# Optimization experiments

Measured on AMD Instinct MI355X. Metric: run time of the kernel, lower is better.

The kernel has to match this reference:

```python
import jax, jax.numpy as jnp
import numpy as np

DIM = 256
NUM_HEADS = 4
HEAD_DIM = DIM // NUM_HEADS


def setup_inputs() -> dict:
    key = jax.random.key(0)
    ks = jax.random.split(key, 8)
    B, N, C = 4, 2048, DIM
    x = jax.random.normal(ks[0], (B, N, C), dtype=jnp.float32)
    R = jax.random.normal(ks[1], (B, 3, 3), dtype=jnp.float32)
    P = jax.random.normal(ks[2], (N, 3), dtype=jnp.float32)
    s = 1.0 / np.sqrt(C)
    qkv_w = jax.random.normal(ks[3], (3 * C, C), dtype=jnp.float32) * s
    qkv_b = jax.random.normal(ks[4], (3 * C,), dtype=jnp.float32) * 0.02
    proj_w = jax.random.normal(ks[5], (C, C), dtype=jnp.float32) * s
    proj_b = jax.random.normal(ks[6], (C,), dtype=jnp.float32) * 0.02
    pos_scale = jnp.asarray(1.0, dtype=jnp.float32)
    return {"x": x, "R": R, "P": P, "qkv_w": qkv_w, "qkv_b": qkv_b,
            "proj_w": proj_w, "proj_b": proj_b, "pos_scale": pos_scale}


def reference(x, R, P, qkv_w, qkv_b, proj_w, proj_b, pos_scale):
    B, N, C = x.shape
    H, D = NUM_HEADS, HEAD_DIM
    scale = D ** -0.5
    # qkv: (B,N,3C) -> (3,B,H,N,D)
    qkv = (x @ qkv_w.T + qkv_b).reshape(B, N, 3, H, D).transpose(2, 0, 3, 1, 4)
    q, k, v = qkv[0], qkv[1], qkv[2]
    # attention logits (B,H,N,N)
    attn = jnp.einsum('bhid,bhjd->bhij', q, k) * scale
    # positional bias: RP = (R @ P^T)^T -> (B,N,3); bias_ij = dot(RP_i, P_j)
    RP = jnp.einsum('bab,jb->bja', R, P) if False else jnp.einsum('bca,ja->bjc', jnp.swapaxes(R, 1, 2), P)
    RP = jnp.einsum('bcd,jd->bjc', R, P)  # (B,N,3): (R @ P.T).T
    bias = jnp.einsum('bik,jk->bij', RP, P)[:, None, :, :] * pos_scale  # (B,1,N,N) broadcast over heads
    attn = jax.nn.softmax(attn + bias, axis=-1)
    out = jnp.einsum('bhij,bhjd->bhid', attn, v)  # (B,H,N,D)
    out = out.transpose(0, 2, 1, 3).reshape(B, N, C)
    out = out @ proj_w.T + proj_b
    return out
```

## Files before the change

### kernel.cpp

```cpp
#include <hip/hip_runtime.h>
#include <hip/hip_bf16.h>

#define B_ 4
#define N_ 2048
#define C_ 256
#define H_ 4
#define D_ 64

typedef __attribute__((ext_vector_type(8))) short bf16x8;
typedef __attribute__((ext_vector_type(4))) float f32x4;

#define LOG2E 1.4426950408889634f

static __device__ inline unsigned short f2bf(float f) {
    unsigned u = __builtin_bit_cast(unsigned, f);
    unsigned r = (u + 0x7fffu + ((u >> 16) & 1u)) >> 16;
    return (unsigned short)r;
}
static __device__ inline float bf2f(unsigned short h) {
    unsigned u = ((unsigned)h) << 16;
    return __builtin_bit_cast(float, u);
}
static __device__ inline unsigned pack2(float a, float b) {
    __hip_bfloat162 h = __float22bfloat162_rn(make_float2(a, b));
    unsigned u;
    __builtin_memcpy(&u, &h, 4);
    return u;
}
static __device__ inline bf16x8 ld_frag(const unsigned short* p) {
    return __builtin_bit_cast(bf16x8, *(const uint4*)p);
}
static __device__ inline void gload_lds16(const unsigned short* g, unsigned short* l) {
    __builtin_amdgcn_global_load_lds(
        (const __attribute__((address_space(1))) unsigned int*)(g),
        (__attribute__((address_space(3))) unsigned int*)(l),
        16, 0, 0);
}
template<int CTRL>
static __device__ inline float fmax_dpp(float x) {
    int yi = __builtin_amdgcn_update_dpp(0, __builtin_bit_cast(int, x),
                                         CTRL, 0xf, 0xf, true);
    return fmaxf(x, __builtin_bit_cast(float, yi));
}

__global__ __launch_bounds__(256) void cvt_kernel(
    const float* __restrict__ x, const float* __restrict__ qkv_w,
    const float* __restrict__ proj_w, const float* __restrict__ Pm,
    unsigned short* __restrict__ xb, unsigned short* __restrict__ wqb,
    unsigned short* __restrict__ wpb, unsigned short* __restrict__ eb)
{
    const int bid = blockIdx.x, tid = threadIdx.x;
    if (bid >= 1152) {
        const int n = (bid - 1152) * 256 + tid;
        const float* pp = Pm + n * 3;
        float p0 = pp[0], p1 = pp[1], p2 = pp[2];
        unsigned u0 = f2bf(p0), u1 = f2bf(p1), u2 = f2bf(p2);
        unsigned v0 = f2bf(p0 - bf2f((unsigned short)u0));
        unsigned v1 = f2bf(p1 - bf2f((unsigned short)u1));
        unsigned v2 = f2bf(p2 - bf2f((unsigned short)u2));
        uint4 lo, hi;
        lo.x = u0 | (u1 << 16); lo.y = u2 | (v0 << 16);
        lo.z = v1 | (v2 << 16); lo.w = u0 | (u1 << 16);
        hi.x = u2; hi.y = 0u; hi.z = 0u; hi.w = 0u;
        *(uint4*)&eb[n * 16 + 0] = lo;
        *(uint4*)&eb[n * 16 + 8] = hi;
        return;
    }
    const float* s; unsigned short* d; int i;
    if (bid < 1024)      { s = x;      d = xb;  i = (bid * 256 + tid) * 8; }
    else if (bid < 1120) { s = qkv_w;  d = wqb; i = ((bid - 1024) * 256 + tid) * 8; }
    else                 { s = proj_w; d = wpb; i = ((bid - 1120) * 256 + tid) * 8; }
    float4 a = *(const float4*)(s + i);
    float4 b = *(const float4*)(s + i + 4);
    uint4 u;
    u.x = pack2(a.x, a.y); u.y = pack2(a.z, a.w);
    u.z = pack2(b.x, b.y); u.w = pack2(b.z, b.w);
    *(uint4*)(d + i) = u;
}

__global__ __launch_bounds__(256) void qkv_gemm(
    const unsigned short* __restrict__ xb, const unsigned short* __restrict__ wb,
    const float* __restrict__ bias, unsigned short* __restrict__ qb,
    unsigned short* __restrict__ kb, unsigned short* __restrict__ vt)
{
    __shared__ __align__(16) unsigned short As[128 * 40];
    __shared__ __align__(16) unsigned short Bs[128 * 40];
    const int m0 = blockIdx.x * 128, o0 = blockIdx.y * 128;
    const int tid = threadIdx.x;
    const int wave = tid >> 6, lane = tid & 63, quad = lane >> 4, l16 = lane & 15;
    const int wy = wave >> 1, wx = wave & 1;

    f32x4 acc[4][4];
    #pragma unroll
    for (int i = 0; i < 4; ++i)
        #pragma unroll
        for (int j = 0; j < 4; ++j) acc[i][j] = (f32x4){0.f, 0.f, 0.f, 0.f};

    const int srow = tid >> 1, soff = (tid & 1) * 16;

    for (int k0 = 0; k0 < 256; k0 += 32) {
        __syncthreads();
        {
            const unsigned short* sa = &xb[(size_t)(m0 + srow) * 256 + k0 + soff];
            const unsigned short* sb = &wb[(size_t)(o0 + srow) * 256 + k0 + soff];
            *(uint4*)&As[srow * 40 + soff + 0] = *(const uint4*)(sa + 0);
            *(uint4*)&As[srow * 40 + soff + 8] = *(const uint4*)(sa + 8);
            *(uint4*)&Bs[srow * 40 + soff + 0] = *(const uint4*)(sb + 0);
            *(uint4*)&Bs[srow * 40 + soff + 8] = *(const uint4*)(sb + 8);
        }
        __syncthreads();
        bf16x8 a[4], b[4];
        #pragma unroll
        for (int mt = 0; mt < 4; ++mt) a[mt] = ld_frag(&As[(wy * 64 + mt * 16 + l16) * 40 + quad * 8]);
        #pragma unroll
        for (int nt = 0; nt < 4; ++nt) b[nt] = ld_frag(&Bs[(wx * 64 + nt * 16 + l16) * 40 + quad * 8]);
        #pragma unroll
        for (int mt = 0; mt < 4; ++mt)
            #pragma unroll
            for (int nt = 0; nt < 4; ++nt)
                acc[mt][nt] = __builtin_amdgcn_mfma_f32_16x16x32_bf16(a[mt], b[nt], acc[mt][nt], 0, 0, 0);
    }

    const int sec = o0 + wx * 64;
    const int three = sec >> 8;
    const int h = (sec >> 6) & 3;
    const int b = m0 >> 11;
    float bv[4];
    #pragma unroll
    for (int nt = 0; nt < 4; ++nt) bv[nt] = bias[sec + nt * 16 + l16];

    if (three == 2) {
        const int n64 = (m0 + wy * 64) & 2047;
        const size_t bh64 = ((size_t)b * H_ + h) * 64;
        #pragma unroll
        for (int nt = 0; nt < 4; ++nt) {
            int d = nt * 16 + l16;
            #pragma unroll
            for (int r = 0; r < 4; ++r) {
                ushort4 v;
                v.x = f2bf(acc[0][nt][r] + bv[nt]);
                v.y = f2bf(acc[1][nt][r] + bv[nt]);
                v.z = f2bf(acc[2][nt][r] + bv[nt]);
                v.w = f2bf(acc[3][nt][r] + bv[nt]);
                *(ushort4*)&vt[(bh64 + d) * N_ + n64 + 16 * quad + 4 * r] = v;
            }
        }
    } else {
        unsigned short* dst = (three == 0) ? qb : kb;
        float sc = (three == 0) ? (0.125f * LOG2E) : 1.0f;
        #pragma unroll
        for (int mt = 0; mt < 4; ++mt)
            #pragma unroll
            for (int r = 0; r < 4; ++r) {
                int n = (m0 + wy * 64 + mt * 16 + quad * 4 + r) & 2047;
                size_t rowbase = (((size_t)b * H_ + h) * N_ + n) * D_;
                #pragma unroll
                for (int nt = 0; nt < 4; ++nt)
                    dst[rowbase + nt * 16 + l16] = f2bf((acc[mt][nt][r] + bv[nt]) * sc);
            }
    }
}

#define LDK 64

__global__ __launch_bounds__(256) void attn_kernel(
    const unsigned short* __restrict__ qb, const unsigned short* __restrict__ kb,
    const unsigned short* __restrict__ vt, const unsigned short* __restrict__ eb,
    const float* __restrict__ Rm, const float* __restrict__ Pm,
    const float* __restrict__ ps_ptr,
    unsigned short* __restrict__ Opart, float* __restrict__ ml)
{
    __shared__ __align__(16) unsigned short Ks[2][64 * LDK];
    __shared__ __align__(16) unsigned short Vs[2][64 * LDK];
    __shared__ __align__(16) unsigned short Ps[64 * LDK];

    const int bh = blockIdx.y;
    const int b = bh >> 2;
    const int i0 = blockIdx.x * 64;
    const int split = blockIdx.z;
    const int tid = threadIdx.x;
    const int wave = tid >> 6, lane = tid & 63;
    const int quad = lane >> 4, l16 = lane & 15;
    const int x7 = l16 & 7;
    const float ps = ps_ptr[0];

    const size_t base = (size_t)bh * N_ * D_;
    const unsigned short* qg = qb + base;
    const unsigned short* kg = kb + base;
    const unsigned short* vg = vt + base;

    const int jbeg = split * (N_ / 4);

    const int rl = lane >> 3, sl = lane & 7;
    const int swz = (sl ^ rl) * 8;
    const unsigned short* kq = kg + (size_t)(jbeg + wave * 16 + rl) * D_ + swz;
    const unsigned short* vq = vg + (size_t)(wave * 16 + rl) * N_ + jbeg + swz;
    const unsigned short* ep = eb + (size_t)(jbeg + l16) * 16 + (quad & 1) * 8;

    auto ISSUE_K = [&](int nb) {
        unsigned short* kd = &Ks[nb][(wave * 16) * LDK];
        gload_lds16(kq,          kd);
        gload_lds16(kq + 8 * D_, kd + 8 * LDK);
        kq += 64 * D_;
    };
    auto ISSUE_V = [&](int nb) {
        unsigned short* vd = &Vs[nb][(wave * 16) * LDK];
        gload_lds16(vq,          vd);
        gload_lds16(vq + 8 * N_, vd + 8 * LDK);
        vq += 64;
    };
    auto LOAD_E = [&](bf16x8 (&e)[4]) {
        #pragma unroll
        for (int t = 0; t < 4; ++t) e[t] = ld_frag(ep + t * 256);
        ep += 64 * 16;
    };

    ISSUE_K(0);
    bf16x8 eA[4], eB[4];
    LOAD_E(eA);

    const int qrow = i0 + wave * 16 + l16;
    bf16x8 aq[3];
    #pragma unroll
    for (int ks = 0; ks < 2; ++ks)
        aq[ks] = ld_frag(&qg[(size_t)qrow * D_ + ks * 32 + quad * 8]);

    {
        float p0 = Pm[qrow * 3 + 0], p1 = Pm[qrow * 3 + 1], p2 = Pm[qrow * 3 + 2];
        float sc = ps * LOG2E;
        unsigned short ah[3], al[3];
        #pragma unroll
        for (int c = 0; c < 3; ++c) {
            float a = (Rm[b * 9 + c * 3 + 0] * p0 + Rm[b * 9 + c * 3 + 1] * p1
                     + Rm[b * 9 + c * 3 + 2] * p2) * sc;
            ah[c] = f2bf(a);
            al[c] = f2bf(a - bf2f(ah[c]));
        }
        bf16x8 e = (bf16x8){0,0,0,0,0,0,0,0};
        if (quad == 0) {
            e[0] = (short)ah[0]; e[1] = (short)ah[1]; e[2] = (short)ah[2];
            e[3] = (short)ah[0]; e[4] = (short)ah[1]; e[5] = (short)ah[2];
            e[6] = (short)al[0]; e[7] = (short)al[1];
        } else if (quad == 1) {
            e[0] = (short)al[2];
        }
        aq[2] = e;
    }

    const bf16x8 ones = (bf16x8){0x3F80,0x3F80,0x3F80,0x3F80,0x3F80,0x3F80,0x3F80,0x3F80};

    float m_run = -1e30f;
    f32x4 o_acc[4], lacc;
    #pragma unroll
    for (int t = 0; t < 4; ++t) o_acc[t] = (f32x4){0.f, 0.f, 0.f, 0.f};
    lacc = (f32x4){0.f, 0.f, 0.f, 0.f};

    f32x4 sA[4], sB[4];

    auto S_COMPUTE = [&](f32x4 (&sc)[4], int kb_, bf16x8 (&ec)[4]) {
        __builtin_amdgcn_s_setprio(1);
        #pragma unroll
        for (int t = 0; t < 4; ++t) {
            const int rb = (l16 + 16 * t) * LDK;
            f32x4 c = {0.f, 0.f, 0.f, 0.f};
            #pragma unroll
            for (int ks = 0; ks < 2; ++ks) {
                bf16x8 bk = ld_frag(&Ks[kb_][rb + (((ks * 4 + quad) ^ x7) * 8)]);
                c = __builtin_amdgcn_mfma_f32_16x16x32_bf16(aq[ks], bk, c, 0, 0, 0);
            }
            c = __builtin_amdgcn_mfma_f32_16x16x32_bf16(aq[2], ec[t], c, 0, 0, 0);
            sc[t] = c;
        }
        __builtin_amdgcn_s_setprio(0);
    };

    auto SOFTMAX = [&](f32x4 (&s)[4]) {
        float mt[4];
        #pragma unroll
        for (int t = 0; t < 4; ++t)
            mt[t] = fmaxf(fmaxf(s[t][0], s[t][1]), fmaxf(s[t][2], s[t][3]));
        float mx = fmaxf(fmaxf(mt[0], mt[1]), fmaxf(mt[2], mt[3]));
        mx = fmax_dpp<0xB1>(mx);
        mx = fmax_dpp<0x4E>(mx);
        mx = fmax_dpp<0x124>(mx);
        mx = fmax_dpp<0x128>(mx);
        if (__any(mx > m_run + 8.0f)) {
            float mnew = fmaxf(m_run, mx);
            float alpha = exp2f(m_run - mnew);
            #pragma unroll
            for (int t = 0; t < 4; ++t)
                #pragma unroll
                for (int r = 0; r < 4; ++r)
                    o_acc[t][r] *= alpha;
            #pragma unroll
            for (int r = 0; r < 4; ++r) lacc[r] *= alpha;
            m_run = mnew;
        }
        #pragma unroll
        for (int r = 0; r < 4; ++r) {
            float p0 = exp2f(s[0][r] - m_run), p1 = exp2f(s[1][r] - m_run);
            float p2 = exp2f(s[2][r] - m_run), p3 = exp2f(s[3][r] - m_run);
            uint2 w;
            w.x = pack2(p0, p1);
            w.y = pack2(p2, p3);
            const int prow = quad * 4 + r;
            *(uint2*)&Ps[(wave * 16 + prow) * LDK
                         + (((l16 >> 1) ^ (prow & 7)) * 8) + (l16 & 1) * 4] = w;
        }
    };

    auto PV = [&](int vb_) {
        __builtin_amdgcn_s_setprio(1);
        #pragma unroll
        for (int ks = 0; ks < 2; ++ks) {
            bf16x8 ap = ld_frag(&Ps[(wave * 16 + l16) * LDK
                                    + (((ks * 4 + quad) ^ x7) * 8)]);
            #pragma unroll
            for (int t = 0; t < 4; ++t) {
                bf16x8 bv = ld_frag(&Vs[vb_][(l16 + 16 * t) * LDK
                                             + (((ks * 4 + quad) ^ x7) * 8)]);
                o_acc[t] = __builtin_amdgcn_mfma_f32_16x16x32_bf16(ap, bv, o_acc[t], 0, 0, 0);
            }
            lacc = __builtin_amdgcn_mfma_f32_16x16x32_bf16(ap, ones, lacc, 0, 0, 0);
        }
        __builtin_amdgcn_s_setprio(0);
    };

    auto STEP = [&](int cur, bool more, f32x4 (&snew)[4], f32x4 (&sold)[4],
                    bf16x8 (&euse)[4], bf16x8 (&eload)[4]) {
        asm volatile("s_waitcnt vmcnt(0)" ::: "memory");
        __builtin_amdgcn_s_barrier();
        __builtin_amdgcn_sched_barrier(0);
        if (more) ISSUE_K(cur ^ 1);
        ISSUE_V(cur);
        SOFTMAX(sold);
        S_COMPUTE(snew, cur, euse);
        if (more) LOAD_E(eload);
        PV(cur ^ 1);
    };

    asm volatile("s_waitcnt vmcnt(0)" ::: "memory");
    __builtin_amdgcn_s_barrier();
    __builtin_amdgcn_sched_barrier(0);
    ISSUE_K(1);
    ISSUE_V(0);
    S_COMPUTE(sA, 0, eA);
    LOAD_E(eB);

    #pragma unroll 1
    for (int it = 0; it < 3; ++it) {
        STEP(1, true, sB, sA, eB, eA);
        STEP(0, true, sA, sB, eA, eB);
    }
    STEP(1, false, sB, sA, eB, eA);

    asm volatile("s_waitcnt vmcnt(0)" ::: "memory");
    __builtin_amdgcn_s_barrier();
    __builtin_amdgcn_sched_barrier(0);
    SOFTMAX(sB);
    PV(1);

    const size_t pbase = (size_t)(split * 16 + bh) * N_;
    #pragma unroll
    for (int r = 0; r < 4; ++r) {
        int row = i0 + wave * 16 + quad * 4 + r;
        #pragma unroll
        for (int t = 0; t < 4; ++t)
            Opart[(pbase + row) * D_ + l16 + 16 * t] = f2bf(o_acc[t][r]);
        if (l16 == 0) {
            float2* mlp = (float2*)ml;
            mlp[pbase + row] = make_float2(m_run, lacc[r]);
        }
    }
}

__global__ __launch_bounds__(256) void proj_gemm(
    const unsigned short* __restrict__ Opart, const float* __restrict__ ml,
    const unsigned short* __restrict__ wb, const float* __restrict__ bias,
    float* __restrict__ out)
{
    __shared__ __align__(16) unsigned short As[64 * 40];
    __shared__ __align__(16) unsigned short Bs[64 * 40];
    const int m0 = blockIdx.x * 64, o0 = blockIdx.y * 64;
    const int tid = threadIdx.x;
    const int wave = tid >> 6, lane = tid & 63, quad = lane >> 4, l16 = lane & 15;
    const float2* mlp = (const float2*)ml;

    const int srow = tid >> 2, scb = (tid & 3) * 8;
    const int sm = m0 + srow, sb = sm >> 11, sn = sm & 2047;

    float wgt[4][4];
    #pragma unroll
    for (int h = 0; h < 4; ++h) {
        size_t r1 = (size_t)(sb * 4 + h) * N_ + sn;
        float2 m0v = mlp[r1], m1v = mlp[r1 + 16 * N_];
        float2 m2v = mlp[r1 + 32 * N_], m3v = mlp[r1 + 48 * N_];
        float mm = fmaxf(fmaxf(m0v.x, m1v.x), fmaxf(m2v.x, m3v.x));
        float w0 = exp2f(m0v.x - mm), w1 = exp2f(m1v.x - mm);
        float w2 = exp2f(m2v.x - mm), w3 = exp2f(m3v.x - mm);
        float inv = 1.f / (m0v.y * w0 + m1v.y * w1 + m2v.y * w2 + m3v.y * w3);
        wgt[h][0] = w0 * inv; wgt[h][1] = w1 * inv;
        wgt[h][2] = w2 * inv; wgt[h][3] = w3 * inv;
    }

    f32x4 acc[4];
    #pragma unroll
    for (int j = 0; j < 4; ++j) acc[j] = (f32x4){0.f, 0.f, 0.f, 0.f};

    for (int k0 = 0; k0 < 256; k0 += 32) {
        const int h = k0 >> 6;
        const int d0 = (k0 & 63) + scb;
        __syncthreads();
        {
            size_t r1 = (size_t)(sb * 4 + h) * N_ + sn;
            union { uint4 u; unsigned short s[8]; } a0, a1, a2, a3;
            a0.u = *(const uint4*)&Opart[(r1 +  0 * N_) * D_ + d0];
            a1.u = *(const uint4*)&Opart[(r1 + 16 * N_) * D_ + d0];
            a2.u = *(const uint4*)&Opart[(r1 + 32 * N_) * D_ + d0];
            a3.u = *(const uint4*)&Opart[(r1 + 48 * N_) * D_ + d0];
            float w0 = wgt[h][0], w1 = wgt[h][1], w2 = wgt[h][2], w3 = wgt[h][3];
            uint4 mv;
            unsigned* mp = (unsigned*)&mv;
            #pragma unroll
            for (int j = 0; j < 4; ++j) {
                float lo = bf2f(a0.s[2*j]) * w0 + bf2f(a1.s[2*j]) * w1
                         + bf2f(a2.s[2*j]) * w2 + bf2f(a3.s[2*j]) * w3;
                float hi = bf2f(a0.s[2*j+1]) * w0 + bf2f(a1.s[2*j+1]) * w1
                         + bf2f(a2.s[2*j+1]) * w2 + bf2f(a3.s[2*j+1]) * w3;
                mp[j] = pack2(lo, hi);
            }
            *(uint4*)&As[srow * 40 + scb] = mv;
            *(uint4*)&Bs[srow * 40 + scb] = *(const uint4*)&wb[(size_t)(o0 + srow) * 256 + k0 + scb];
        }
        __syncthreads();
        bf16x8 a = ld_frag(&As[(wave * 16 + l16) * 40 + quad * 8]);
        #pragma unroll
        for (int nt = 0; nt < 4; ++nt) {
            bf16x8 b = ld_frag(&Bs[(nt * 16 + l16) * 40 + quad * 8]);
            acc[nt] = __builtin_amdgcn_mfma_f32_16x16x32_bf16(a, b, acc[nt], 0, 0, 0);
        }
    }

    float bv[4];
    #pragma unroll
    for (int nt = 0; nt < 4; ++nt) bv[nt] = bias[o0 + nt * 16 + l16];
    #pragma unroll
    for (int r = 0; r < 4; ++r) {
        int m = m0 + wave * 16 + quad * 4 + r;
        #pragma unroll
        for (int nt = 0; nt < 4; ++nt)
            out[(size_t)m * 256 + o0 + nt * 16 + l16] = acc[nt][r] + bv[nt];
    }
}

extern "C" void kernel_launch(void* const* d_in, const int* in_sizes, int n_in,
                              void* d_out, int out_size, void* d_ws, size_t ws_size,
                              hipStream_t stream) {
    const float* x       = (const float*)d_in[0];
    const float* Rm      = (const float*)d_in[1];
    const float* Pm      = (const float*)d_in[2];
    const float* qkv_w   = (const float*)d_in[3];
    const float* qkv_b   = (const float*)d_in[4];
    const float* proj_w  = (const float*)d_in[5];
    const float* proj_b  = (const float*)d_in[6];
    const float* pos_scl = (const float*)d_in[7];
    float* out = (float*)d_out;

    const size_t NE = (size_t)B_ * H_ * N_ * D_;
    unsigned short* opart = (unsigned short*)d_ws;
    unsigned short* qb    = opart + 4 * NE;
    unsigned short* kb    = qb   + NE;
    unsigned short* vtb   = kb   + NE;
    float*          mlb   = (float*)(vtb + NE);
    unsigned short* eb    = (unsigned short*)(mlb + (size_t)4 * 16 * N_ * 2);
    unsigned short* wqb   = eb  + 2048 * 16;
    unsigned short* wpb   = wqb + 768 * 256;
    unsigned short* xb    = opart;

    cvt_kernel<<<1160, 256, 0, stream>>>(x, qkv_w, proj_w, Pm, xb, wqb, wpb, eb);
    qkv_gemm<<<dim3(64, 6), 256, 0, stream>>>(xb, wqb, qkv_b, qb, kb, vtb);
    attn_kernel<<<dim3(32, 16, 4), 256, 0, stream>>>(qb, kb, vtb, eb, Rm, Pm, pos_scl, opart, mlb);
    proj_gemm<<<dim3(128, 4), 256, 0, stream>>>(opart, mlb, wpb, proj_b, out);
}
```

Before: 136.2 us.

## Double-buffer QKV and projection GEMMs with direct-to-LDS loads and XOR swizzle

Rewrites the K loops of the QKV and output-projection GEMMs to use double-buffered shared memory with a K step of 64. Tiles are fetched via global-to-LDS direct loads into an XOR-swizzled layout, so the next tile's fetch overlaps MFMA work on the current one and bank conflicts are avoided. The projection kernel also prefetches the next head's partial outputs into registers. The cost is double the LDS footprint and more register pressure, and the gains are limited to the two GEMM stages; the attention kernel is untouched.

New measurement: 134.3 us. Within noise of the previous version (-1.4%).

```diff
diff --git a/kernel.cpp b/kernel.cpp
--- a/kernel.cpp
+++ b/kernel.cpp
@@ -83,12 +83,28 @@
     const float* __restrict__ bias, unsigned short* __restrict__ qb,
     unsigned short* __restrict__ kb, unsigned short* __restrict__ vt)
 {
-    __shared__ __align__(16) unsigned short As[128 * 40];
-    __shared__ __align__(16) unsigned short Bs[128 * 40];
+    __shared__ __align__(16) unsigned short As[2][128 * 64];
+    __shared__ __align__(16) unsigned short Bs[2][128 * 64];
     const int m0 = blockIdx.x * 128, o0 = blockIdx.y * 128;
     const int tid = threadIdx.x;
     const int wave = tid >> 6, lane = tid & 63, quad = lane >> 4, l16 = lane & 15;
     const int wy = wave >> 1, wx = wave & 1;
+    const int x7 = l16 & 7;
+    const int rl = lane >> 3, sl = lane & 7;
+    const int swz = (sl ^ rl) * 8;
+
+    const unsigned short* aq0 = &xb[(size_t)(m0 + 32 * wave + rl) * 256 + swz];
+    const unsigned short* bq0 = &wb[(size_t)(o0 + 32 * wave + rl) * 256 + swz];
+
+    auto ISSUE = [&](int buf, int k0) {
+        unsigned short* ad = &As[buf][(32 * wave) * 64];
+        unsigned short* bd = &Bs[buf][(32 * wave) * 64];
+        #pragma unroll
+        for (int i = 0; i < 4; ++i) {
+            gload_lds16(aq0 + (size_t)(8 * i) * 256 + k0, ad + (8 * i) * 64);
+            gload_lds16(bq0 + (size_t)(8 * i) * 256 + k0, bd + (8 * i) * 64);
+        }
+    };
 
     f32x4 acc[4][4];
     #pragma unroll
@@ -96,29 +112,34 @@
         #pragma unroll
         for (int j = 0; j < 4; ++j) acc[i][j] = (f32x4){0.f, 0.f, 0.f, 0.f};
 
-    const int srow = tid >> 1, soff = (tid & 1) * 16;
-
-    for (int k0 = 0; k0 < 256; k0 += 32) {
-        __syncthreads();
-        {
-            const unsigned short* sa = &xb[(size_t)(m0 + srow) * 256 + k0 + soff];
-            const unsigned short* sb = &wb[(size_t)(o0 + srow) * 256 + k0 + soff];
-            *(uint4*)&As[srow * 40 + soff + 0] = *(const uint4*)(sa + 0);
-            *(uint4*)&As[srow * 40 + soff + 8] = *(const uint4*)(sa + 8);
-            *(uint4*)&Bs[srow * 40 + soff + 0] = *(const uint4*)(sb + 0);
-            *(uint4*)&Bs[srow * 40 + soff + 8] = *(const uint4*)(sb + 8);
-        }
-        __syncthreads();
-        bf16x8 a[4], b[4];
-        #pragma unroll
-        for (int mt = 0; mt < 4; ++mt) a[mt] = ld_frag(&As[(wy * 64 + mt * 16 + l16) * 40 + quad * 8]);
-        #pragma unroll
-        for (int nt = 0; nt < 4; ++nt) b[nt] = ld_frag(&Bs[(wx * 64 + nt * 16 + l16) * 40 + quad * 8]);
-        #pragma unroll
-        for (int mt = 0; mt < 4; ++mt)
+    ISSUE(0, 0);
+
+    #pragma unroll
+    for (int t = 0; t < 4; ++t) {
+        const int cur = t & 1;
+        asm volatile("s_waitcnt vmcnt(0)" ::: "memory");
+        __builtin_amdgcn_s_barrier();
+        __builtin_amdgcn_sched_barrier(0);
+        if (t < 3) ISSUE(cur ^ 1, (t + 1) * 64);
+        __builtin_amdgcn_s_setprio(1);
+        #pragma unroll
+        for (int ks = 0; ks < 2; ++ks) {
+            bf16x8 a[4], b[4];
+            #pragma unroll
+            for (int mt = 0; mt < 4; ++mt)
+                a[mt] = ld_frag(&As[cur][(wy * 64 + mt * 16 + l16) * 64
+                                         + (((ks * 4 + quad) ^ x7) * 8)]);
             #pragma unroll
             for (int nt = 0; nt < 4; ++nt)
-                acc[mt][nt] = __builtin_amdgcn_mfma_f32_16x16x32_bf16(a[mt], b[nt], acc[mt][nt], 0, 0, 0);
+                b[nt] = ld_frag(&Bs[cur][(wx * 64 + nt * 16 + l16) * 64
+                                         + (((ks * 4 + quad) ^ x7) * 8)]);
+            #pragma unroll
+            for (int mt = 0; mt < 4; ++mt)
+                #pragma unroll
+                for (int nt = 0; nt < 4; ++nt)
+                    acc[mt][nt] = __builtin_amdgcn_mfma_f32_16x16x32_bf16(a[mt], b[nt], acc[mt][nt], 0, 0, 0);
+        }
+        __builtin_amdgcn_s_setprio(0);
     }
 
     const int sec = o0 + wx * 64;
@@ -379,14 +400,18 @@
     const unsigned short* __restrict__ wb, const float* __restrict__ bias,
     float* __restrict__ out)
 {
-    __shared__ __align__(16) unsigned short As[64 * 40];
-    __shared__ __align__(16) unsigned short Bs[64 * 40];
+    __shared__ __align__(16) unsigned short As[2][64 * 64];
+    __shared__ __align__(16) unsigned short Bs[2][64 * 64];
     const int m0 = blockIdx.x * 64, o0 = blockIdx.y * 64;
     const int tid = threadIdx.x;
     const int wave = tid >> 6, lane = tid & 63, quad = lane >> 4, l16 = lane & 15;
+    const int x7 = l16 & 7;
+    const int rl = lane >> 3, sl = lane & 7;
+    const int swz = (sl ^ rl) * 8;
     const float2* mlp = (const float2*)ml;
 
-    const int srow = tid >> 2, scb = (tid & 3) * 8;
+    const int srow = tid >> 2, sc16 = (tid & 3) * 16;
+    const int s0 = (tid & 3) * 2;
     const int sm = m0 + srow, sb = sm >> 11, sn = sm & 2047;
 
     float wgt[4][4];
@@ -403,42 +428,70 @@
         wgt[h][2] = w2 * inv; wgt[h][3] = w3 * inv;
     }
 
+    const unsigned short* bq0 = &wb[(size_t)(o0 + 16 * wave + rl) * 256 + swz];
+    auto ISSUE_B = [&](int buf, int k0) {
+        unsigned short* bd = &Bs[buf][(16 * wave) * 64];
+        gload_lds16(bq0 + k0,           bd);
+        gload_lds16(bq0 + 8 * 256 + k0, bd + 8 * 64);
+    };
+
+    union U16 { uint4 u; unsigned short s[8]; };
+    U16 ar[4][2];
+    auto LOAD_A = [&](int h) {
+        size_t r1 = (size_t)(sb * 4 + h) * N_ + sn;
+        #pragma unroll
+        for (int s = 0; s < 4; ++s) {
+            const unsigned short* p = &Opart[(r1 + (size_t)(16 * s) * N_) * D_ + sc16];
+            ar[s][0].u = *(const uint4*)(p);
+            ar[s][1].u = *(const uint4*)(p + 8);
+        }
+    };
+
+    ISSUE_B(0, 0);
+    LOAD_A(0);
+
     f32x4 acc[4];
     #pragma unroll
     for (int j = 0; j < 4; ++j) acc[j] = (f32x4){0.f, 0.f, 0.f, 0.f};
 
-    for (int k0 = 0; k0 < 256; k0 += 32) {
-        const int h = k0 >> 6;
-        const int d0 = (k0 & 63) + scb;
+    #pragma unroll
+    for (int t = 0; t < 4; ++t) {
+        const int cur = t & 1;
+        {
+            float w0 = wgt[t][0], w1 = wgt[t][1], w2 = wgt[t][2], w3 = wgt[t][3];
+            #pragma unroll
+            for (int j = 0; j < 2; ++j) {
+                uint4 mv;
+                unsigned* mp = (unsigned*)&mv;
+                #pragma unroll
+                for (int q = 0; q < 4; ++q) {
+                    float lo = bf2f(ar[0][j].s[2*q])   * w0 + bf2f(ar[1][j].s[2*q])   * w1
+                             + bf2f(ar[2][j].s[2*q])   * w2 + bf2f(ar[3][j].s[2*q])   * w3;
+                    float hi = bf2f(ar[0][j].s[2*q+1]) * w0 + bf2f(ar[1][j].s[2*q+1]) * w1
+                             + bf2f(ar[2][j].s[2*q+1]) * w2 + bf2f(ar[3][j].s[2*q+1]) * w3;
+                    mp[q] = pack2(lo, hi);
+                }
+                *(uint4*)&As[cur][srow * 64 + (((s0 + j) ^ (srow & 7)) * 8)] = mv;
+            }
+        }
         __syncthreads();
-        {
-            size_t r1 = (size_t)(sb * 4 + h) * N_ + sn;
-            union { uint4 u; unsigned short s[8]; } a0, a1, a2, a3;
-            a0.u = *(const uint4*)&Opart[(r1 +  0 * N_) * D_ + d0];
-            a1.u = *(const uint4*)&Opart[(r1 + 16 * N_) * D_ + d0];
-            a2.u = *(const uint4*)&Opart[(r1 + 32 * N_) * D_ + d0];
-            a3.u = *(const uint4*)&Opart[(r1 + 48 * N_) * D_ + d0];
-            float w0 = wgt[h][0], w1 = wgt[h][1], w2 = wgt[h][2], w3 = wgt[h][3];
-            uint4 mv;
-            unsigned* mp = (unsigned*)&mv;
-            #pragma unroll
-            for (int j = 0; j < 4; ++j) {
-                float lo = bf2f(a0.s[2*j]) * w0 + bf2f(a1.s[2*j]) * w1
-                         + bf2f(a2.s[2*j]) * w2 + bf2f(a3.s[2*j]) * w3;
-                float hi = bf2f(a0.s[2*j+1]) * w0 + bf2f(a1.s[2*j+1]) * w1
-                         + bf2f(a2.s[2*j+1]) * w2 + bf2f(a3.s[2*j+1]) * w3;
-                mp[j] = pack2(lo, hi);
+        if (t < 3) {
+            ISSUE_B(cur ^ 1, (t + 1) * 64);
+            LOAD_A(t + 1);
+        }
+        __builtin_amdgcn_s_setprio(1);
+        #pragma unroll
+        for (int ks = 0; ks < 2; ++ks) {
+            bf16x8 a = ld_frag(&As[cur][(wave * 16 + l16) * 64
+                                        + (((ks * 4 + quad) ^ x7) * 8)]);
+            #pragma unroll
+            for (int nt = 0; nt < 4; ++nt) {
+                bf16x8 b = ld_frag(&Bs[cur][(nt * 16 + l16) * 64
+                                            + (((ks * 4 + quad) ^ x7) * 8)]);
+                acc[nt] = __builtin_amdgcn_mfma_f32_16x16x32_bf16(a, b, acc[nt], 0, 0, 0);
             }
-            *(uint4*)&As[srow * 40 + scb] = mv;
-            *(uint4*)&Bs[srow * 40 + scb] = *(const uint4*)&wb[(size_t)(o0 + srow) * 256 + k0 + scb];
-        }
-        __syncthreads();
-        bf16x8 a = ld_frag(&As[(wave * 16 + l16) * 40 + quad * 8]);
-        #pragma unroll
-        for (int nt = 0; nt < 4; ++nt) {
-            bf16x8 b = ld_frag(&Bs[(nt * 16 + l16) * 40 + quad * 8]);
-            acc[nt] = __builtin_amdgcn_mfma_f32_16x16x32_bf16(a, b, acc[nt], 0, 0, 0);
-        }
+        }
+        __builtin_amdgcn_s_setprio(0);
     }
 
     float bv[4];
```
